# Kernel optimization log

Hardware: AMD Instinct MI355X
Metric: run time of the kernel (lower is better)

The kernel has to match this reference:

```python
import jax, jax.numpy as jnp
import numpy as np

B, C_IN, C_INT, C_OUT, H, W = 4, 1024, 256, 1024, 64, 64
EPS = 1e-5

def conv1x1(x, w, b):
    # x: (B, Cin, H, W), w: (Cout, Cin), b: (Cout,)
    return jnp.einsum('bchw,oc->bohw', x, w) + b[None, :, None, None]

def batchnorm_eval(x, gamma, beta, mean, var):
    inv = gamma / jnp.sqrt(var + EPS)
    return x * inv[None, :, None, None] + (beta - mean * inv)[None, :, None, None]

def setup_inputs() -> dict:
    key = jax.random.key(0)
    ks = jax.random.split(key, 8)
    s_in = 1.0 / np.sqrt(C_IN)
    s_int = 1.0 / np.sqrt(C_INT)
    return {
        'x': jax.random.normal(ks[0], (B, C_IN, H, W), dtype=jnp.float32),
        'w_key': jax.random.normal(ks[1], (C_INT, C_IN), dtype=jnp.float32) * s_in,
        'b_key': jnp.zeros((C_INT,), dtype=jnp.float32),
        'gamma': jnp.ones((C_INT,), dtype=jnp.float32),
        'beta': jnp.zeros((C_INT,), dtype=jnp.float32),
        'mean': jnp.zeros((C_INT,), dtype=jnp.float32),
        'var': jnp.ones((C_INT,), dtype=jnp.float32),
        'w_value': jax.random.normal(ks[2], (C_INT, C_IN), dtype=jnp.float32) * s_in,
        'b_value': jax.random.normal(ks[3], (C_INT,), dtype=jnp.float32) * 0.1,
        'w_out': jax.random.normal(ks[4], (C_OUT, C_INT), dtype=jnp.float32) * s_int,
        'b_out': jax.random.normal(ks[5], (C_OUT,), dtype=jnp.float32) * 0.1,
    }

def reference(x, w_key, b_key, gamma, beta, mean, var, w_value, b_value, w_out, b_out):
    Bb, _, h, w = x.shape
    N = h * w
    # value: 1x1 conv, (B, C, N) -> (B, N, C)
    value = conv1x1(x, w_value, b_value).reshape(Bb, C_INT, N).transpose(0, 2, 1)
    # query/key share the same conv+BN (f_query = f_key)
    qk = batchnorm_eval(conv1x1(x, w_key, b_key), gamma, beta, mean, var).reshape(Bb, C_INT, N)
    query = qk.transpose(0, 2, 1)  # (B, N, C)
    key = qk                        # (B, C, N)
    sim = jnp.einsum('bnc,bcm->bnm', query, key) * (C_INT ** -0.5)  # (B, N, N)
    sim = jax.nn.softmax(sim, axis=-1)
    context = jnp.einsum('bnm,bmc->bnc', sim, value)  # (B, N, C)
    context = context.transpose(0, 2, 1).reshape(Bb, C_INT, h, w)
    return conv1x1(context, w_out, b_out)
```

## Files before the change

kernel.cpp:

```cpp
#include <hip/hip_runtime.h>

#define BATCH 4
#define CIN   1024
#define CI    256
#define CO    1024
#define NSP   4096

typedef __attribute__((ext_vector_type(8))) short bf16x8;
typedef __attribute__((ext_vector_type(4))) float f32x4;
typedef __attribute__((ext_vector_type(2))) unsigned uint2v;

struct __align__(8) us4 { unsigned short x, y, z, w; };

#define DEVI __device__ __forceinline__

DEVI unsigned short f2bf(float f) {
  union { float f; unsigned u; } un; un.f = f;
  unsigned u = un.u;
  u += 0x7FFFu + ((u >> 16) & 1u);
  return (unsigned short)(u >> 16);
}

DEVI unsigned cvtpk(float lo, float hi) {
  unsigned r;
  asm("v_cvt_pk_bf16_f32 %0, %1, %2" : "=v"(r) : "v"(lo), "v"(hi));
  return r;
}

DEVI void gl2lds16(const void* g, void* l) {
  __builtin_amdgcn_global_load_lds(
      (const __attribute__((address_space(1))) void*)g,
      (__attribute__((address_space(3))) void*)l, 16, 0, 0);
}

DEVI f32x4 mfma16(bf16x8 a, bf16x8 b, f32x4 c) {
  return __builtin_amdgcn_mfma_f32_16x16x32_bf16(a, b, c, 0, 0, 0);
}

__global__ __launch_bounds__(256) void k_prep(
    const float* __restrict__ w_key, const float* __restrict__ w_val,
    const float* __restrict__ w_out,
    const float* __restrict__ gamma, const float* __restrict__ beta,
    const float* __restrict__ mean,  const float* __restrict__ var,
    const float* __restrict__ b_key,
    unsigned short* __restrict__ wkv, unsigned short* __restrict__ wob,
    float* __restrict__ sq, float* __restrict__ bq)
{
  int idx = blockIdx.x * 256 + threadIdx.x;
  float wv = (idx < 262144) ? w_key[idx] : w_val[idx - 262144];
  wkv[idx] = f2bf(wv);
  if (idx < 262144) wob[idx] = f2bf(w_out[idx]);
  if (idx < 256) {
    float inv = gamma[idx] * rsqrtf(var[idx] + 1e-5f);
    sq[idx] = 0.25f * inv;
    bq[idx] = 0.25f * (beta[idx] + (b_key[idx] - mean[idx]) * inv);
  }
}

__global__ __launch_bounds__(256) void k_xpose(const float* __restrict__ x,
                                               unsigned short* __restrict__ xT)
{
  __shared__ unsigned short tile[64][66];
  int b = blockIdx.z, k0 = blockIdx.y * 64, n0 = blockIdx.x * 64;
  int tid = threadIdx.x;
  int rr = tid >> 4, cc = tid & 15;
  const float* xb = x + ((size_t)b * CIN + k0) * NSP + n0;
#pragma unroll
  for (int p = 0; p < 4; ++p) {
    int row = p * 16 + rr;
    float4 v = *(const float4*)(xb + (size_t)row * NSP + cc * 4);
    *(unsigned*)&tile[row][cc * 4 + 0] = cvtpk(v.x, v.y);
    *(unsigned*)&tile[row][cc * 4 + 2] = cvtpk(v.z, v.w);
  }
  __syncthreads();
  unsigned short* xtb = xT + ((size_t)b * NSP + n0) * CIN + k0;
#pragma unroll
  for (int p = 0; p < 4; ++p) {
    int n = p * 16 + rr;
    int kq = cc * 4;
    us4 pk;
    pk.x = tile[kq + 0][n]; pk.y = tile[kq + 1][n];
    pk.z = tile[kq + 2][n]; pk.w = tile[kq + 3][n];
    *(us4*)(xtb + (size_t)n * CIN + kq) = pk;
  }
}

template<int KDIM>
DEVI void gemm_core(const unsigned short* __restrict__ Ab,
                    const unsigned short* __restrict__ Bb,
                    unsigned short* ldsA, unsigned short* ldsB,
                    f32x4 acc[4][4], int tid)
{
  const int lane = tid & 63, wave = tid >> 6;
  const int q = lane >> 4, ln = lane & 15;
  const int wm = wave & 1, wn = wave >> 1;

  int aoff[4][2], boff[4][2];
#pragma unroll
  for (int f = 0; f < 4; ++f) {
    int ra = wm * 64 + f * 16 + ln;
    aoff[f][0] = (ra * 8 + ((q)     ^ (ra & 7))) * 8;
    aoff[f][1] = (ra * 8 + ((q + 4) ^ (ra & 7))) * 8;
    int rb = wn * 64 + f * 16 + ln;
    boff[f][0] = (rb * 8 + ((q)     ^ (rb & 7))) * 8;
    boff[f][1] = (rb * 8 + ((q + 4) ^ (rb & 7))) * 8;
  }
  int sgo[4];
#pragma unroll
  for (int i = 0; i < 4; ++i) {
    int s = i * 256 + tid;
    int row = s >> 3;
    int c8 = (s & 7) ^ (row & 7);
    sgo[i] = row * KDIM + c8 * 8;
  }
  for (int k0 = 0; k0 < KDIM; k0 += 64) {
#pragma unroll
    for (int i = 0; i < 4; ++i) {
      gl2lds16(Ab + sgo[i] + k0, ldsA + (i * 256 + wave * 64) * 8);
      gl2lds16(Bb + sgo[i] + k0, ldsB + (i * 256 + wave * 64) * 8);
    }
    __syncthreads();
#pragma unroll
    for (int kk = 0; kk < 2; ++kk) {
      bf16x8 af[4], bfr[4];
#pragma unroll
      for (int f = 0; f < 4; ++f) af[f]  = *(const bf16x8*)(ldsA + aoff[f][kk]);
#pragma unroll
      for (int f = 0; f < 4; ++f) bfr[f] = *(const bf16x8*)(ldsB + boff[f][kk]);
#pragma unroll
      for (int mf = 0; mf < 4; ++mf)
#pragma unroll
        for (int nf = 0; nf < 4; ++nf)
          acc[mf][nf] = mfma16(af[mf], bfr[nf], acc[mf][nf]);
    }
    __syncthreads();
  }
}

template<int KDIM>
DEVI void gemm_core_db(const unsigned short* __restrict__ Ab,
                       const unsigned short* __restrict__ Bb,
                       unsigned short* ldsA, unsigned short* ldsB,
                       f32x4 acc[4][4], int tid)
{
  const int lane = tid & 63, wave = tid >> 6;
  const int q = lane >> 4, ln = lane & 15;
  const int wm = wave & 1, wn = wave >> 1;

  int aoff[4][2], boff[4][2];
#pragma unroll
  for (int f = 0; f < 4; ++f) {
    int ra = wm * 64 + f * 16 + ln;
    aoff[f][0] = (ra * 8 + ((q)     ^ (ra & 7))) * 8;
    aoff[f][1] = (ra * 8 + ((q + 4) ^ (ra & 7))) * 8;
    int rb = wn * 64 + f * 16 + ln;
    boff[f][0] = (rb * 8 + ((q)     ^ (rb & 7))) * 8;
    boff[f][1] = (rb * 8 + ((q + 4) ^ (rb & 7))) * 8;
  }
  int sgo[4];
#pragma unroll
  for (int i = 0; i < 4; ++i) {
    int s = i * 256 + tid;
    int row = s >> 3;
    int c8 = (s & 7) ^ (row & 7);
    sgo[i] = row * KDIM + c8 * 8;
  }
#pragma unroll
  for (int i = 0; i < 4; ++i) {
    gl2lds16(Ab + sgo[i], ldsA + (i * 256 + wave * 64) * 8);
    gl2lds16(Bb + sgo[i], ldsB + (i * 256 + wave * 64) * 8);
  }
  __syncthreads();

  for (int k0 = 0; k0 < KDIM; k0 += 64) {
    const int cur = (k0 >> 6) & 1;
    unsigned short* A = ldsA + cur * (128 * 64);
    unsigned short* B = ldsB + cur * (128 * 64);
    if (k0 + 64 < KDIM) {
      unsigned short* An = ldsA + (cur ^ 1) * (128 * 64);
      unsigned short* Bn = ldsB + (cur ^ 1) * (128 * 64);
#pragma unroll
      for (int i = 0; i < 4; ++i) {
        gl2lds16(Ab + sgo[i] + k0 + 64, An + (i * 256 + wave * 64) * 8);
        gl2lds16(Bb + sgo[i] + k0 + 64, Bn + (i * 256 + wave * 64) * 8);
      }
    }
#pragma unroll
    for (int kk = 0; kk < 2; ++kk) {
      bf16x8 af[4], bfr[4];
#pragma unroll
      for (int f = 0; f < 4; ++f) af[f]  = *(const bf16x8*)(A + aoff[f][kk]);
#pragma unroll
      for (int f = 0; f < 4; ++f) bfr[f] = *(const bf16x8*)(B + boff[f][kk]);
#pragma unroll
      for (int mf = 0; mf < 4; ++mf)
#pragma unroll
        for (int nf = 0; nf < 4; ++nf)
          acc[mf][nf] = mfma16(af[mf], bfr[nf], acc[mf][nf]);
    }
    __syncthreads();
  }
}

__global__ __launch_bounds__(256) void k_convqkv(
    const unsigned short* __restrict__ wkv,
    const unsigned short* __restrict__ xT,
    const float* __restrict__ sq, const float* __restrict__ bq,
    const float* __restrict__ bval,
    unsigned short* __restrict__ qkT,
    unsigned short* __restrict__ vv)
{
  __shared__ __align__(16) unsigned short ldsA[2 * 128 * 64];
  __shared__ __align__(16) unsigned short ldsB[2 * 128 * 64];
  int b = blockIdx.z, m0 = blockIdx.y * 128, n0 = blockIdx.x * 128;
  int tid = threadIdx.x;
  f32x4 z = {0.f, 0.f, 0.f, 0.f};
  f32x4 acc[4][4];
#pragma unroll
  for (int i = 0; i < 4; ++i)
#pragma unroll
    for (int j = 0; j < 4; ++j) acc[i][j] = z;

  gemm_core_db<CIN>(wkv + (size_t)m0 * CIN, xT + ((size_t)b * NSP + n0) * CIN,
                    ldsA, ldsB, acc, tid);

  int lane = tid & 63, wave = tid >> 6, q = lane >> 4, ln = lane & 15;
  int wm = wave & 1, wn = wave >> 1;
  if (m0 < 256) {
#pragma unroll
    for (int mf = 0; mf < 4; ++mf) {
      int cb = m0 + wm * 64 + mf * 16 + q * 4;
      float s0_ = sq[cb + 0], s1_ = sq[cb + 1], s2_ = sq[cb + 2], s3_ = sq[cb + 3];
      float b0_ = bq[cb + 0], b1_ = bq[cb + 1], b2_ = bq[cb + 2], b3_ = bq[cb + 3];
#pragma unroll
      for (int nf = 0; nf < 4; ++nf) {
        int n = n0 + wn * 64 + nf * 16 + ln;
        us4 pk;
        pk.x = f2bf(acc[mf][nf][0] * s0_ + b0_);
        pk.y = f2bf(acc[mf][nf][1] * s1_ + b1_);
        pk.z = f2bf(acc[mf][nf][2] * s2_ + b2_);
        pk.w = f2bf(acc[mf][nf][3] * s3_ + b3_);
        *(us4*)(qkT + ((size_t)b * NSP + n) * CI + cb) = pk;
      }
    }
  } else {
#pragma unroll
    for (int mf = 0; mf < 4; ++mf) {
      int cb = (m0 - 256) + wm * 64 + mf * 16 + q * 4;
#pragma unroll
      for (int r = 0; r < 4; ++r) {
        float bv = bval[cb + r];
#pragma unroll
        for (int nf = 0; nf < 4; ++nf) {
          int n = n0 + wn * 64 + nf * 16 + ln;
          vv[((size_t)b * CI + (cb + r)) * NSP + n] = f2bf(acc[mf][nf][r] + bv);
        }
      }
    }
  }
}

__global__ __launch_bounds__(256, 2) void k_attn_part(
    const unsigned short* __restrict__ qkT,
    const unsigned short* __restrict__ vv,
    unsigned* __restrict__ Opart,
    float* __restrict__ Lpart)
{
  __shared__ __align__(16) unsigned short Kt[2][32 * 256];
  __shared__ __align__(16) unsigned short Vt[2][256 * 32];
  __shared__ __align__(16) unsigned short Pl[4 * 32 * 40];

  int bid = blockIdx.x;
  int slice = bid & 15, qt = bid >> 4;
  int b = slice >> 2, js = slice & 3;
  int n0 = qt * 128;
  int tid = threadIdx.x, lane = tid & 63, wave = tid >> 6;
  int q = lane >> 4, ln = lane & 15;
  const unsigned short* qkb = qkT + (size_t)b * NSP * CI;
  const unsigned short* vb  = vv  + (size_t)b * CI * NSP;

  bf16x8 Qf0[8], Qf1[8];
  {
    const unsigned short* qr0 = qkb + (size_t)(n0 + wave * 32 + ln) * CI + q * 8;
    const unsigned short* qr1 = qr0 + 16 * CI;
#pragma unroll
    for (int t = 0; t < 8; ++t) Qf0[t] = *(const bf16x8*)(qr0 + t * 32);
#pragma unroll
    for (int t = 0; t < 8; ++t) Qf1[t] = *(const bf16x8*)(qr1 + t * 32);
  }

  int kbA = (ln * 32 + ((q ^ (ln & 7)) & 7)) * 8;
  int kbB = (ln * 32 + (((4 + q) ^ (ln & 7)) & 7)) * 8;
  int vbase = (ln * 4 + ((q ^ ((ln >> 1) & 3)) & 3)) * 8;

  unsigned short* Plw = Pl + wave * (32 * 40);
  int pw0 = ln * 40 + q * 4;
  int pw1 = ln * 40 + 16 + q * 4;
  int pw2 = (ln + 16) * 40 + q * 4;
  int pw3 = (ln + 16) * 40 + 16 + q * 4;
  int pr0 = ln * 40 + q * 8;
  int pr1 = (ln + 16) * 40 + q * 8;

  int gko[4], gvo[4];
#pragma unroll
  for (int i = 0; i < 4; ++i) {
    int s = i * 256 + tid;
    int j = s >> 5, f = s & 31;
    gko[i] = j * CI + ((f & 24) | ((f ^ j) & 7)) * 8;
    int c = s >> 2;
    gvo[i] = c * NSP + ((s ^ (c >> 1)) & 3) * 8;
  }

  f32x4 O0[16], O1[16];
  f32x4 z = {0.f, 0.f, 0.f, 0.f};
#pragma unroll
  for (int cf = 0; cf < 16; ++cf) { O0[cf] = z; O1[cf] = z; }
  float l0c = 0.f, l1c = 0.f;

  int jbase = js * 1024;

#pragma unroll
  for (int i = 0; i < 4; ++i)
    gl2lds16(qkb + (size_t)jbase * CI + gko[i], &Kt[0][(i * 256 + wave * 64) * 8]);
#pragma unroll
  for (int i = 0; i < 4; ++i)
    gl2lds16(vb + jbase + gvo[i], &Vt[0][(i * 256 + wave * 64) * 8]);
  __syncthreads();

  for (int it = 0; it < 32; ++it) {
    int cur = it & 1;

    if (it < 31) {
      int j1 = jbase + (it + 1) * 32;
#pragma unroll
      for (int i = 0; i < 4; ++i)
        gl2lds16(qkb + (size_t)j1 * CI + gko[i],
                 &Kt[cur ^ 1][(i * 256 + wave * 64) * 8]);
#pragma unroll
      for (int i = 0; i < 4; ++i)
        gl2lds16(vb + j1 + gvo[i],
                 &Vt[cur ^ 1][(i * 256 + wave * 64) * 8]);
    }

    const unsigned short* Kc = Kt[cur];
    const unsigned short* Vc = Vt[cur];

    f32x4 s0 = z, s1 = z, s2 = z, s3 = z;
    __builtin_amdgcn_s_setprio(1);
#pragma unroll
    for (int t = 0; t < 8; ++t) {
      int ko = ((t & 1) ? kbB : kbA) + (t >> 1) * 64;
      bf16x8 kf0 = *(const bf16x8*)(Kc + ko);
      bf16x8 kf1 = *(const bf16x8*)(Kc + ko + 4096);
      s0 = mfma16(kf0, Qf0[t], s0);
      s1 = mfma16(kf1, Qf0[t], s1);
      s2 = mfma16(kf0, Qf1[t], s2);
      s3 = mfma16(kf1, Qf1[t], s3);
    }
    __builtin_amdgcn_s_setprio(0);

    float p00 = __expf(s0[0]), p01 = __expf(s0[1]);
    float p02 = __expf(s0[2]), p03 = __expf(s0[3]);
    float p04 = __expf(s1[0]), p05 = __expf(s1[1]);
    float p06 = __expf(s1[2]), p07 = __expf(s1[3]);
    float p10 = __expf(s2[0]), p11 = __expf(s2[1]);
    float p12 = __expf(s2[2]), p13 = __expf(s2[3]);
    float p14 = __expf(s3[0]), p15 = __expf(s3[1]);
    float p16 = __expf(s3[2]), p17 = __expf(s3[3]);

    uint2v w;
    w.x = cvtpk(p00, p01); w.y = cvtpk(p02, p03);
    *(uint2v*)(Plw + pw0) = w;
    w.x = cvtpk(p04, p05); w.y = cvtpk(p06, p07);
    *(uint2v*)(Plw + pw1) = w;
    w.x = cvtpk(p10, p11); w.y = cvtpk(p12, p13);
    *(uint2v*)(Plw + pw2) = w;
    w.x = cvtpk(p14, p15); w.y = cvtpk(p16, p17);
    *(uint2v*)(Plw + pw3) = w;

    l0c += ((p00 + p01) + (p02 + p03)) + ((p04 + p05) + (p06 + p07));
    l1c += ((p10 + p11) + (p12 + p13)) + ((p14 + p15) + (p16 + p17));

    bf16x8 pf0 = *(const bf16x8*)(Plw + pr0);
    bf16x8 pf1 = *(const bf16x8*)(Plw + pr1);
    __builtin_amdgcn_s_setprio(1);
#pragma unroll
    for (int cf = 0; cf < 16; ++cf) {
      bf16x8 vf = *(const bf16x8*)(Vc + vbase + cf * 512);
      O0[cf] = mfma16(pf0, vf, O0[cf]);
      O1[cf] = mfma16(pf1, vf, O1[cf]);
    }
    __builtin_amdgcn_s_setprio(0);

    __syncthreads();
  }

  l0c += __shfl_xor(l0c, 16); l0c += __shfl_xor(l0c, 32);
  l1c += __shfl_xor(l1c, 16); l1c += __shfl_xor(l1c, 32);

  unsigned* Ob = Opart + (size_t)bid * (64 * 256);
  if (lane < 16) {
    Lpart[bid * 128 + wave * 32 + lane] = l0c;
    Lpart[bid * 128 + wave * 32 + 16 + lane] = l1c;
  }
#pragma unroll
  for (int r = 0; r < 4; ++r) {
    int rp = wave * 16 + q * 4 + r;
#pragma unroll
    for (int cf = 0; cf < 16; ++cf)
      Ob[rp * 256 + cf * 16 + ln] = cvtpk(O0[cf][r], O1[cf][r]);
  }
}

__global__ __launch_bounds__(256) void k_merge(
    const unsigned* __restrict__ Opart,
    const float* __restrict__ Lpart,
    unsigned short* __restrict__ ctx)
{
  __shared__ float Winv[64];
  int mb = blockIdx.x;
  int b = mb >> 6, qg = mb & 63;
  int qt = qg >> 1, half = qg & 1;
  int tid = threadIdx.x;
  int pb0 = qt * 16 + b * 4;

  if (tid < 64) {
    int row = half * 64 + tid;
    float L = Lpart[(pb0 + 0) * 128 + row]
            + Lpart[(pb0 + 1) * 128 + row]
            + Lpart[(pb0 + 2) * 128 + row]
            + Lpart[(pb0 + 3) * 128 + row];
    Winv[tid] = 1.0f / L;
  }
  __syncthreads();

  const unsigned* P0 = Opart + ((size_t)(pb0 + 0) * 64 + half * 32) * 256;
  const unsigned* P1 = Opart + ((size_t)(pb0 + 1) * 64 + half * 32) * 256;
  const unsigned* P2 = Opart + ((size_t)(pb0 + 2) * 64 + half * 32) * 256;
  const unsigned* P3 = Opart + ((size_t)(pb0 + 3) * 64 + half * 32) * 256;
  unsigned short* cb = ctx + ((size_t)b * NSP + qg * 64) * CI;
#pragma unroll 4
  for (int rp = 0; rp < 32; ++rp) {
    unsigned u0 = P0[rp * 256 + tid], u1 = P1[rp * 256 + tid];
    unsigned u2 = P2[rp * 256 + tid], u3 = P3[rp * 256 + tid];
    float lo = __uint_as_float(u0 << 16) + __uint_as_float(u1 << 16)
             + __uint_as_float(u2 << 16) + __uint_as_float(u3 << 16);
    float hi = __uint_as_float(u0 & 0xFFFF0000u) + __uint_as_float(u1 & 0xFFFF0000u)
             + __uint_as_float(u2 & 0xFFFF0000u) + __uint_as_float(u3 & 0xFFFF0000u);
    int ra = (rp & 15) + ((rp >> 4) << 5);
    int rb = ra + 16;
    cb[(size_t)ra * CI + tid] = f2bf(lo * Winv[ra]);
    cb[(size_t)rb * CI + tid] = f2bf(hi * Winv[rb]);
  }
}

__global__ __launch_bounds__(256) void k_convout(
    const unsigned short* __restrict__ wo,
    const unsigned short* __restrict__ ctx,
    const float* __restrict__ bout,
    float* __restrict__ out)
{
  __shared__ __align__(16) unsigned short ldsA[128 * 64];
  __shared__ __align__(16) unsigned short ldsB[128 * 64];
  int b = blockIdx.z, m0 = blockIdx.y * 128, n0 = blockIdx.x * 128;
  int tid = threadIdx.x;
  f32x4 z = {0.f, 0.f, 0.f, 0.f};
  f32x4 acc[4][4];
#pragma unroll
  for (int i = 0; i < 4; ++i)
#pragma unroll
    for (int j = 0; j < 4; ++j) acc[i][j] = z;

  gemm_core<CI>(wo + (size_t)m0 * CI, ctx + ((size_t)b * NSP + n0) * CI,
                ldsA, ldsB, acc, tid);

  int lane = tid & 63, wave = tid >> 6, q = lane >> 4, ln = lane & 15;
  int wm = wave & 1, wn = wave >> 1;
#pragma unroll
  for (int mf = 0; mf < 4; ++mf) {
    int cb = m0 + wm * 64 + mf * 16 + q * 4;
    float bo0 = bout[cb + 0], bo1 = bout[cb + 1], bo2 = bout[cb + 2], bo3 = bout[cb + 3];
#pragma unroll
    for (int nf = 0; nf < 4; ++nf) {
      int n = n0 + wn * 64 + nf * 16 + ln;
      float* p = out + ((size_t)b * CO + cb) * NSP + n;
      p[0 * (size_t)NSP] = acc[mf][nf][0] + bo0;
      p[1 * (size_t)NSP] = acc[mf][nf][1] + bo1;
      p[2 * (size_t)NSP] = acc[mf][nf][2] + bo2;
      p[3 * (size_t)NSP] = acc[mf][nf][3] + bo3;
    }
  }
}

extern "C" void kernel_launch(void* const* d_in, const int* in_sizes, int n_in,
                              void* d_out, int out_size, void* d_ws, size_t ws_size,
                              hipStream_t stream) {
  const float* x     = (const float*)d_in[0];
  const float* w_key = (const float*)d_in[1];
  const float* b_key = (const float*)d_in[2];
  const float* gamma = (const float*)d_in[3];
  const float* beta  = (const float*)d_in[4];
  const float* mean  = (const float*)d_in[5];
  const float* var   = (const float*)d_in[6];
  const float* w_val = (const float*)d_in[7];
  const float* b_val = (const float*)d_in[8];
  const float* w_out = (const float*)d_in[9];
  const float* b_out = (const float*)d_in[10];
  float* out = (float*)d_out;

  char* ws = (char*)d_ws;
  unsigned short* xT  = (unsigned short*)(ws);
  unsigned short* wkv = (unsigned short*)(ws + 33554432);
  unsigned short* wob = (unsigned short*)(ws + 34603008);
  unsigned short* qkT = (unsigned short*)(ws + 35127296);
  unsigned short* vv  = (unsigned short*)(ws + 43515904);
  unsigned short* ctx = (unsigned short*)(ws + 51904512);
  float* sq = (float*)(ws + 60293120);
  float* bq = (float*)(ws + 60294144);
  unsigned* Opart = (unsigned*)(ws + 60295168);
  float* Lpart = (float*)(ws + 127404032);

  k_prep<<<2048, 256, 0, stream>>>(w_key, w_val, w_out, gamma, beta, mean, var,
                                   b_key, wkv, wob, sq, bq);
  k_xpose<<<dim3(64, 16, 4), 256, 0, stream>>>(x, xT);
  k_convqkv<<<dim3(32, 4, 4), 256, 0, stream>>>(wkv, xT, sq, bq, b_val, qkT, vv);
  k_attn_part<<<512, 256, 0, stream>>>(qkT, vv, Opart, Lpart);
  k_merge<<<256, 256, 0, stream>>>(Opart, Lpart, ctx);
  k_convout<<<dim3(32, 8, 4), 256, 0, stream>>>(wob, ctx, b_out, out);
}
```

Measured before the change: 262.2 us.

## Fuse prep and transpose kernels, widen convout tile, coalesce value stores

```diff
diff --git a/kernel.cpp b/kernel.cpp
--- a/kernel.cpp
+++ b/kernel.cpp
@@ -37,7 +37,8 @@
   return __builtin_amdgcn_mfma_f32_16x16x32_bf16(a, b, c, 0, 0, 0);
 }
 
-__global__ __launch_bounds__(256) void k_prep(
+__global__ __launch_bounds__(256) void k_xpose_prep(
+    const float* __restrict__ x, unsigned short* __restrict__ xT,
     const float* __restrict__ w_key, const float* __restrict__ w_val,
     const float* __restrict__ w_out,
     const float* __restrict__ gamma, const float* __restrict__ beta,
@@ -46,22 +47,22 @@
     unsigned short* __restrict__ wkv, unsigned short* __restrict__ wob,
     float* __restrict__ sq, float* __restrict__ bq)
 {
-  int idx = blockIdx.x * 256 + threadIdx.x;
-  float wv = (idx < 262144) ? w_key[idx] : w_val[idx - 262144];
-  wkv[idx] = f2bf(wv);
-  if (idx < 262144) wob[idx] = f2bf(w_out[idx]);
-  if (idx < 256) {
-    float inv = gamma[idx] * rsqrtf(var[idx] + 1e-5f);
-    sq[idx] = 0.25f * inv;
-    bq[idx] = 0.25f * (beta[idx] + (b_key[idx] - mean[idx]) * inv);
-  }
-}
-
-__global__ __launch_bounds__(256) void k_xpose(const float* __restrict__ x,
-                                               unsigned short* __restrict__ xT)
-{
+  int bid = blockIdx.x;
+  if (bid < 2048) {
+    int idx = bid * 256 + threadIdx.x;
+    float wv = (idx < 262144) ? w_key[idx] : w_val[idx - 262144];
+    wkv[idx] = f2bf(wv);
+    if (idx < 262144) wob[idx] = f2bf(w_out[idx]);
+    if (idx < 256) {
+      float inv = gamma[idx] * rsqrtf(var[idx] + 1e-5f);
+      sq[idx] = 0.25f * inv;
+      bq[idx] = 0.25f * (beta[idx] + (b_key[idx] - mean[idx]) * inv);
+    }
+    return;
+  }
   __shared__ unsigned short tile[64][66];
-  int b = blockIdx.z, k0 = blockIdx.y * 64, n0 = blockIdx.x * 64;
+  int id2 = bid - 2048;
+  int b = id2 >> 10, k0 = ((id2 >> 6) & 15) * 64, n0 = (id2 & 63) * 64;
   int tid = threadIdx.x;
   int rr = tid >> 4, cc = tid & 15;
   const float* xb = x + ((size_t)b * CIN + k0) * NSP + n0;
@@ -86,10 +87,10 @@
 }
 
 template<int KDIM>
-DEVI void gemm_core(const unsigned short* __restrict__ Ab,
-                    const unsigned short* __restrict__ Bb,
-                    unsigned short* ldsA, unsigned short* ldsB,
-                    f32x4 acc[4][4], int tid)
+DEVI void gemm_core_db(const unsigned short* __restrict__ Ab,
+                       const unsigned short* __restrict__ Bb,
+                       unsigned short* ldsA, unsigned short* ldsB,
+                       f32x4 acc[4][4], int tid)
 {
   const int lane = tid & 63, wave = tid >> 6;
   const int q = lane >> 4, ln = lane & 15;
@@ -113,58 +114,6 @@
     int c8 = (s & 7) ^ (row & 7);
     sgo[i] = row * KDIM + c8 * 8;
   }
-  for (int k0 = 0; k0 < KDIM; k0 += 64) {
-#pragma unroll
-    for (int i = 0; i < 4; ++i) {
-      gl2lds16(Ab + sgo[i] + k0, ldsA + (i * 256 + wave * 64) * 8);
-      gl2lds16(Bb + sgo[i] + k0, ldsB + (i * 256 + wave * 64) * 8);
-    }
-    __syncthreads();
-#pragma unroll
-    for (int kk = 0; kk < 2; ++kk) {
-      bf16x8 af[4], bfr[4];
-#pragma unroll
-      for (int f = 0; f < 4; ++f) af[f]  = *(const bf16x8*)(ldsA + aoff[f][kk]);
-#pragma unroll
-      for (int f = 0; f < 4; ++f) bfr[f] = *(const bf16x8*)(ldsB + boff[f][kk]);
-#pragma unroll
-      for (int mf = 0; mf < 4; ++mf)
-#pragma unroll
-        for (int nf = 0; nf < 4; ++nf)
-          acc[mf][nf] = mfma16(af[mf], bfr[nf], acc[mf][nf]);
-    }
-    __syncthreads();
-  }
-}
-
-template<int KDIM>
-DEVI void gemm_core_db(const unsigned short* __restrict__ Ab,
-                       const unsigned short* __restrict__ Bb,
-                       unsigned short* ldsA, unsigned short* ldsB,
-                       f32x4 acc[4][4], int tid)
-{
-  const int lane = tid & 63, wave = tid >> 6;
-  const int q = lane >> 4, ln = lane & 15;
-  const int wm = wave & 1, wn = wave >> 1;
-
-  int aoff[4][2], boff[4][2];
-#pragma unroll
-  for (int f = 0; f < 4; ++f) {
-    int ra = wm * 64 + f * 16 + ln;
-    aoff[f][0] = (ra * 8 + ((q)     ^ (ra & 7))) * 8;
-    aoff[f][1] = (ra * 8 + ((q + 4) ^ (ra & 7))) * 8;
-    int rb = wn * 64 + f * 16 + ln;
-    boff[f][0] = (rb * 8 + ((q)     ^ (rb & 7))) * 8;
-    boff[f][1] = (rb * 8 + ((q + 4) ^ (rb & 7))) * 8;
-  }
-  int sgo[4];
-#pragma unroll
-  for (int i = 0; i < 4; ++i) {
-    int s = i * 256 + tid;
-    int row = s >> 3;
-    int c8 = (s & 7) ^ (row & 7);
-    sgo[i] = row * KDIM + c8 * 8;
-  }
 #pragma unroll
   for (int i = 0; i < 4; ++i) {
     gl2lds16(Ab + sgo[i], ldsA + (i * 256 + wave * 64) * 8);
@@ -202,6 +151,69 @@
   }
 }
 
+DEVI void gemm256(const unsigned short* __restrict__ Ab,
+                  const unsigned short* __restrict__ Bb,
+                  unsigned short* ldsA,
+                  unsigned short* ldsB,
+                  f32x4 acc[8][4], int tid)
+{
+  const int lane = tid & 63, wave = tid >> 6;
+  const int q = lane >> 4, ln = lane & 15;
+  const int wm = wave & 1, wn = wave >> 1;
+
+  int aoff[8][2], boff[4][2];
+#pragma unroll
+  for (int f = 0; f < 8; ++f) {
+    int ra = wm * 128 + f * 16 + ln;
+    aoff[f][0] = (ra * 8 + ((q)     ^ (ra & 7))) * 8;
+    aoff[f][1] = (ra * 8 + ((q + 4) ^ (ra & 7))) * 8;
+  }
+#pragma unroll
+  for (int f = 0; f < 4; ++f) {
+    int rb = wn * 64 + f * 16 + ln;
+    boff[f][0] = (rb * 8 + ((q)     ^ (rb & 7))) * 8;
+    boff[f][1] = (rb * 8 + ((q + 4) ^ (rb & 7))) * 8;
+  }
+  int sgoA[8], sgoB[4];
+#pragma unroll
+  for (int i = 0; i < 8; ++i) {
+    int s = i * 256 + tid;
+    int row = s >> 3;
+    int c8 = (s & 7) ^ (row & 7);
+    sgoA[i] = row * CI + c8 * 8;
+  }
+#pragma unroll
+  for (int i = 0; i < 4; ++i) {
+    int s = i * 256 + tid;
+    int row = s >> 3;
+    int c8 = (s & 7) ^ (row & 7);
+    sgoB[i] = row * CI + c8 * 8;
+  }
+  for (int k0 = 0; k0 < CI; k0 += 64) {
+#pragma unroll
+    for (int i = 0; i < 8; ++i)
+      gl2lds16(Ab + sgoA[i] + k0, ldsA + (i * 256 + wave * 64) * 8);
+#pragma unroll
+    for (int i = 0; i < 4; ++i)
+      gl2lds16(Bb + sgoB[i] + k0, ldsB + (i * 256 + wave * 64) * 8);
+    __syncthreads();
+#pragma unroll
+    for (int kk = 0; kk < 2; ++kk) {
+      bf16x8 af[8], bfr[4];
+#pragma unroll
+      for (int f = 0; f < 8; ++f) af[f]  = *(const bf16x8*)(ldsA + aoff[f][kk]);
+#pragma unroll
+      for (int f = 0; f < 4; ++f) bfr[f] = *(const bf16x8*)(ldsB + boff[f][kk]);
+#pragma unroll
+      for (int mf = 0; mf < 8; ++mf)
+#pragma unroll
+        for (int nf = 0; nf < 4; ++nf)
+          acc[mf][nf] = mfma16(af[mf], bfr[nf], acc[mf][nf]);
+    }
+    __syncthreads();
+  }
+}
+
 __global__ __launch_bounds__(256) void k_convqkv(
     const unsigned short* __restrict__ wkv,
     const unsigned short* __restrict__ xT,
@@ -221,12 +233,14 @@
 #pragma unroll
     for (int j = 0; j < 4; ++j) acc[i][j] = z;
 
-  gemm_core_db<CIN>(wkv + (size_t)m0 * CIN, xT + ((size_t)b * NSP + n0) * CIN,
-                    ldsA, ldsB, acc, tid);
+  const unsigned short* wp = wkv + (size_t)m0 * CIN;
+  const unsigned short* xp = xT + ((size_t)b * NSP + n0) * CIN;
+  bool qk = (m0 < 256);
+  gemm_core_db<CIN>(qk ? wp : xp, qk ? xp : wp, ldsA, ldsB, acc, tid);
 
   int lane = tid & 63, wave = tid >> 6, q = lane >> 4, ln = lane & 15;
   int wm = wave & 1, wn = wave >> 1;
-  if (m0 < 256) {
+  if (qk) {
 #pragma unroll
     for (int mf = 0; mf < 4; ++mf) {
       int cb = m0 + wm * 64 + mf * 16 + q * 4;
@@ -235,26 +249,25 @@
 #pragma unroll
       for (int nf = 0; nf < 4; ++nf) {
         int n = n0 + wn * 64 + nf * 16 + ln;
-        us4 pk;
-        pk.x = f2bf(acc[mf][nf][0] * s0_ + b0_);
-        pk.y = f2bf(acc[mf][nf][1] * s1_ + b1_);
-        pk.z = f2bf(acc[mf][nf][2] * s2_ + b2_);
-        pk.w = f2bf(acc[mf][nf][3] * s3_ + b3_);
-        *(us4*)(qkT + ((size_t)b * NSP + n) * CI + cb) = pk;
+        uint2v pk2;
+        pk2.x = cvtpk(acc[mf][nf][0] * s0_ + b0_, acc[mf][nf][1] * s1_ + b1_);
+        pk2.y = cvtpk(acc[mf][nf][2] * s2_ + b2_, acc[mf][nf][3] * s3_ + b3_);
+        *(uint2v*)(qkT + ((size_t)b * NSP + n) * CI + cb) = pk2;
       }
     }
   } else {
-#pragma unroll
-    for (int mf = 0; mf < 4; ++mf) {
-      int cb = (m0 - 256) + wm * 64 + mf * 16 + q * 4;
-#pragma unroll
-      for (int r = 0; r < 4; ++r) {
-        float bv = bval[cb + r];
-#pragma unroll
-        for (int nf = 0; nf < 4; ++nf) {
-          int n = n0 + wn * 64 + nf * 16 + ln;
-          vv[((size_t)b * CI + (cb + r)) * NSP + n] = f2bf(acc[mf][nf][r] + bv);
-        }
+    int c0 = m0 - 256;
+#pragma unroll
+    for (int nf = 0; nf < 4; ++nf) {
+      int c = c0 + wn * 64 + nf * 16 + ln;
+      float bv = bval[c];
+      unsigned short* vr = vv + ((size_t)b * CI + c) * NSP + n0 + wm * 64 + q * 4;
+#pragma unroll
+      for (int mf = 0; mf < 4; ++mf) {
+        uint2v wv2;
+        wv2.x = cvtpk(acc[mf][nf][0] + bv, acc[mf][nf][1] + bv);
+        wv2.y = cvtpk(acc[mf][nf][2] + bv, acc[mf][nf][3] + bv);
+        *(uint2v*)(vr + mf * 16) = wv2;
       }
     }
   }
@@ -460,25 +473,25 @@
     const float* __restrict__ bout,
     float* __restrict__ out)
 {
-  __shared__ __align__(16) unsigned short ldsA[128 * 64];
+  __shared__ __align__(16) unsigned short ldsA[256 * 64];
   __shared__ __align__(16) unsigned short ldsB[128 * 64];
-  int b = blockIdx.z, m0 = blockIdx.y * 128, n0 = blockIdx.x * 128;
+  int b = blockIdx.z, m0 = blockIdx.y * 256, n0 = blockIdx.x * 128;
   int tid = threadIdx.x;
   f32x4 z = {0.f, 0.f, 0.f, 0.f};
-  f32x4 acc[4][4];
-#pragma unroll
-  for (int i = 0; i < 4; ++i)
+  f32x4 acc[8][4];
+#pragma unroll
+  for (int i = 0; i < 8; ++i)
 #pragma unroll
     for (int j = 0; j < 4; ++j) acc[i][j] = z;
 
-  gemm_core<CI>(wo + (size_t)m0 * CI, ctx + ((size_t)b * NSP + n0) * CI,
-                ldsA, ldsB, acc, tid);
+  gemm256(wo + (size_t)m0 * CI, ctx + ((size_t)b * NSP + n0) * CI,
+          ldsA, ldsB, acc, tid);
 
   int lane = tid & 63, wave = tid >> 6, q = lane >> 4, ln = lane & 15;
   int wm = wave & 1, wn = wave >> 1;
 #pragma unroll
-  for (int mf = 0; mf < 4; ++mf) {
-    int cb = m0 + wm * 64 + mf * 16 + q * 4;
+  for (int mf = 0; mf < 8; ++mf) {
+    int cb = m0 + wm * 128 + mf * 16 + q * 4;
     float bo0 = bout[cb + 0], bo1 = bout[cb + 1], bo2 = bout[cb + 2], bo3 = bout[cb + 3];
 #pragma unroll
     for (int nf = 0; nf < 4; ++nf) {
@@ -520,11 +533,11 @@
   unsigned* Opart = (unsigned*)(ws + 60295168);
   float* Lpart = (float*)(ws + 127404032);
 
-  k_prep<<<2048, 256, 0, stream>>>(w_key, w_val, w_out, gamma, beta, mean, var,
-                                   b_key, wkv, wob, sq, bq);
-  k_xpose<<<dim3(64, 16, 4), 256, 0, stream>>>(x, xT);
+  k_xpose_prep<<<6144, 256, 0, stream>>>(x, xT, w_key, w_val, w_out, gamma,
+                                         beta, mean, var, b_key, wkv, wob,
+                                         sq, bq);
   k_convqkv<<<dim3(32, 4, 4), 256, 0, stream>>>(wkv, xT, sq, bq, b_val, qkT, vv);
   k_attn_part<<<512, 256, 0, stream>>>(qkT, vv, Opart, Lpart);
   k_merge<<<256, 256, 0, stream>>>(Opart, Lpart, ctx);
-  k_convout<<<dim3(32, 8, 4), 256, 0, stream>>>(wob, ctx, b_out, out);
-}
+  k_convout<<<dim3(32, 4, 4), 256, 0, stream>>>(wob, ctx, b_out, out);
+}
```

After: 258.6 us. Within noise of the previous version (-1.4%).
